# Performance work log

Hardware: AMD Instinct MI355X
Metric: run time of the kernel (lower is better)

The kernel has to match this reference:

```python
import jax, jax.numpy as jnp
import numpy as np

MUL = 128            # multiplicity of 0e and 1o node irreps
N_NODES = 10000
N_EDGES = 160000
R_BASIS = 8          # edge_feats_irreps.num_irreps
HIDDEN = 64
W_NUMEL = 4 * MUL    # conv_tp.weight_numel (4 uvu paths, edge mul = 1)
SQRT3 = 3.0 ** 0.5
SILU_2MOM = 1.679177   # e3nn normalize2mom constant for SiLU
AVG_NUM_NEIGHBORS = 10.0


def setup_inputs() -> dict:
    key = jax.random.key(0)
    ks = jax.random.split(key, 12)
    rn = lambda k, s: jax.random.normal(k, s, dtype=jnp.float32)
    return {
        "node_feats": rn(ks[0], (N_NODES, 4 * MUL)),        # 128x0e + 128x1o
        "edge_attrs": rn(ks[1], (N_EDGES, 4)),               # 1x0e + 1x1o spherical harmonics
        "edge_feats": rn(ks[2], (N_EDGES, R_BASIS)),         # 8x0e radial basis
        "edge_index": jax.random.randint(ks[3], (2, N_EDGES), 0, N_NODES),
        "W_up0": rn(ks[4], (MUL, MUL)),                      # linear_up, 0e block
        "W_up1": rn(ks[5], (MUL, MUL)),                      # linear_up, 1o block
        "W_mlp1": rn(ks[6], (R_BASIS, HIDDEN)),
        "W_mlp2": rn(ks[7], (HIDDEN, HIDDEN)),
        "W_mlp3": rn(ks[8], (HIDDEN, HIDDEN)),
        "W_mlp4": rn(ks[9], (HIDDEN, W_NUMEL)),
        "W_out0": rn(ks[10], (2 * MUL, MUL)),                # linear: 256x0e -> 128x0e
        "W_out1": rn(ks[11], (2 * MUL, MUL)),                # linear: 256x1o -> 128x1o
    }


def _lin_irreps(x0, x1, W0, W1):
    # equivariant o3.Linear: per-irrep channel mixing with 1/sqrt(fan_in)
    y0 = (x0 @ W0) / jnp.sqrt(jnp.float32(W0.shape[0]))
    y1 = jnp.einsum('num,uv->nvm', x1, W1) / jnp.sqrt(jnp.float32(W1.shape[0]))
    return y0, y1


def _forward(node_feats, edge_attrs, edge_feats, edge_index,
             W_up0, W_up1, W_mlp1, W_mlp2, W_mlp3, W_mlp4, W_out0, W_out1):
    num_nodes = node_feats.shape[0]
    sender, receiver = edge_index[0], edge_index[1]

    # split node feats into irrep blocks: [N,128] scalars, [N,128,3] vectors
    x0 = node_feats[:, :MUL]
    x1 = node_feats[:, MUL:].reshape(num_nodes, MUL, 3)
    x0, x1 = _lin_irreps(x0, x1, W_up0, W_up1)  # linear_up

    # radial MLP (e3nn FullyConnectedNet with normalized SiLU) -> per-edge TP weights
    h = edge_feats
    for W in (W_mlp1, W_mlp2, W_mlp3):
        h = SILU_2MOM * jax.nn.silu((h @ W) / jnp.sqrt(jnp.float32(W.shape[0])))
    tpw = (h @ W_mlp4) / jnp.sqrt(jnp.float32(W_mlp4.shape[0]))  # [E, 4*MUL]
    w1, w2, w3, w4 = jnp.split(tpw, 4, axis=-1)  # per-path [E, MUL]

    # gather sender features
    s0 = x0[sender]              # [E, MUL]
    s1 = x1[sender]              # [E, MUL, 3]
    y0 = edge_attrs[:, 0:1]      # [E, 1]  (0e sh)
    y1 = edge_attrs[:, 1:4]      # [E, 3]  (1o sh)

    # weighted uvu CG tensor product (component norm: alpha = sqrt(2l_out+1), w3j sum-sq = 1)
    p1 = w1 * s0 * y0                                    # 0e x 0e -> 0e  [E, MUL]
    p2 = (w2 * s0)[:, :, None] * y1[:, None, :]          # 0e x 1o -> 1o  [E, MUL, 3]
    p3 = w3[:, :, None] * s1 * y0[:, None, :]            # 1o x 0e -> 1o  [E, MUL, 3]
    p4 = w4 * jnp.einsum('eum,em->eu', s1, y1) / SQRT3   # 1o x 1o -> 0e  [E, MUL]

    # irreps_mid.simplify() = 256x0e + 256x1o
    m0 = jnp.concatenate([p1, p4], axis=-1)              # [E, 2*MUL]
    m1 = jnp.concatenate([p2, p3], axis=1)               # [E, 2*MUL, 3]

    # scatter-sum over receivers
    msg0 = jax.ops.segment_sum(m0, receiver, num_segments=num_nodes)
    msg1 = jax.ops.segment_sum(m1, receiver, num_segments=num_nodes)

    o0, o1 = _lin_irreps(msg0, msg1, W_out0, W_out1)
    out = jnp.concatenate([o0, o1.reshape(num_nodes, 3 * MUL)], axis=-1)
    return out / AVG_NUM_NEIGHBORS


def reference(node_feats, edge_attrs, edge_feats, edge_index,
              W_up0, W_up1, W_mlp1, W_mlp2, W_mlp3, W_mlp4, W_out0, W_out1):
    return _forward(node_feats, edge_attrs, edge_feats, edge_index,
                    W_up0, W_up1, W_mlp1, W_mlp2, W_mlp3, W_mlp4, W_out0, W_out1)
```

## Files before the change

### kernel.cpp

```cpp
#include <hip/hip_runtime.h>
#include <stdint.h>

#define NN 10000
#define NE 160000

typedef short short8 __attribute__((ext_vector_type(8)));
typedef float f32x4 __attribute__((ext_vector_type(4)));

__device__ __forceinline__ float bf2f(unsigned short u) {
    return __uint_as_float(((uint32_t)u) << 16);
}
__device__ __forceinline__ float bflo(uint32_t u) { return __uint_as_float(u << 16); }
__device__ __forceinline__ float bfhi(uint32_t u) { return __uint_as_float(u & 0xffff0000u); }
__device__ __forceinline__ unsigned short f2bf(float f) {
    uint32_t u = __float_as_uint(f);
    u += 0x7fffu + ((u >> 16) & 1u);
    return (unsigned short)(u >> 16);
}
__device__ __forceinline__ uint32_t pack2(float lo, float hi) {
    return (uint32_t)f2bf(lo) | ((uint32_t)f2bf(hi) << 16);
}
__device__ __forceinline__ float silu2(float x) {
    return 1.679177f * x / (1.f + __expf(-x));
}

__global__ __launch_bounds__(256) void k_wup(const float* __restrict__ Wu0,
                                             const float* __restrict__ Wu1,
                                             unsigned short* __restrict__ w0T,
                                             unsigned short* __restrict__ w1T) {
    const float s = 0.08838834764831845f;
    for (int i = threadIdx.x + blockIdx.x * 256; i < 16384; i += 256 * 64) {
        int u = i >> 7, v = i & 127;
        w0T[v * 128 + u] = f2bf(Wu0[i] * s);
        w1T[v * 128 + u] = f2bf(Wu1[i] * s);
    }
}

__global__ __launch_bounds__(256) void k_prep(const float* __restrict__ nf,
                                              unsigned short* __restrict__ x0b,
                                              unsigned short* __restrict__ x1b) {
    int idx = blockIdx.x * 256 + threadIdx.x;
    int n = idx >> 7, u = idx & 127;
    const float* row = nf + (size_t)n * 512;
    x0b[(size_t)n * 128 + u] = f2bf(row[u]);
    const float* p = row + 128 + u * 3;
    x1b[(size_t)n * 128 + u]                = f2bf(p[0]);
    x1b[1280000 + (size_t)n * 128 + u]      = f2bf(p[1]);
    x1b[2560000 + (size_t)n * 128 + u]      = f2bf(p[2]);
}

__global__ __launch_bounds__(256) void k_upg(const unsigned short* __restrict__ x0b,
                                             const unsigned short* __restrict__ x1b,
                                             const unsigned short* __restrict__ w0T,
                                             const unsigned short* __restrict__ w1T,
                                             float* __restrict__ xw) {
    int wave = threadIdx.x >> 6, lane = threadIdx.x & 63;
    int wid = blockIdx.x * 4 + wave;
    if (wid >= 1250) return;
    int tile = wid >> 1, half = wid & 1;
    int n0 = tile * 16;
    int lm = lane & 15, lq = lane >> 4;

    uint4 A0[4], A1[3][4];
    const unsigned short* a0r = x0b + (size_t)(n0 + lm) * 128 + lq * 8;
#pragma unroll
    for (int kf = 0; kf < 4; ++kf) A0[kf] = *(const uint4*)(a0r + kf * 32);
#pragma unroll
    for (int m = 0; m < 3; ++m) {
        const unsigned short* a1r = x1b + 1280000 * (size_t)m + (size_t)(n0 + lm) * 128 + lq * 8;
#pragma unroll
        for (int kf = 0; kf < 4; ++kf) A1[m][kf] = *(const uint4*)(a1r + kf * 32);
    }

    for (int vq = 0; vq < 4; ++vq) {
        int vt = half * 4 + vq;
        const unsigned short* b0r = w0T + (vt * 16 + lm) * 128 + lq * 8;
        const unsigned short* b1r = w1T + (vt * 16 + lm) * 128 + lq * 8;
        f32x4 acc0 = {0.f, 0.f, 0.f, 0.f};
#pragma unroll
        for (int kf = 0; kf < 4; ++kf) {
            short8 b = __builtin_bit_cast(short8, *(const uint4*)(b0r + kf * 32));
            acc0 = __builtin_amdgcn_mfma_f32_16x16x32_bf16(
                __builtin_bit_cast(short8, A0[kf]), b, acc0, 0, 0, 0);
        }
        f32x4 acc1[3];
#pragma unroll
        for (int m = 0; m < 3; ++m) acc1[m] = (f32x4){0.f, 0.f, 0.f, 0.f};
#pragma unroll
        for (int kf = 0; kf < 4; ++kf) {
            short8 b = __builtin_bit_cast(short8, *(const uint4*)(b1r + kf * 32));
#pragma unroll
            for (int m = 0; m < 3; ++m)
                acc1[m] = __builtin_amdgcn_mfma_f32_16x16x32_bf16(
                    __builtin_bit_cast(short8, A1[m][kf]), b, acc1[m], 0, 0, 0);
        }
        int col = vt * 16 + lm;
#pragma unroll
        for (int r = 0; r < 4; ++r) {
            float* o = xw + (size_t)(n0 + lq * 4 + r) * 512;
            o[col] = acc0[r];
            o[128 + col] = acc1[0][r];
            o[256 + col] = acc1[1][r];
            o[384 + col] = acc1[2][r];
        }
    }
}

__global__ __launch_bounds__(256) void k_wmlp(const float* __restrict__ W1,
                                              const float* __restrict__ W2,
                                              const float* __restrict__ W3,
                                              unsigned short* __restrict__ w1Tp,
                                              unsigned short* __restrict__ w2T,
                                              unsigned short* __restrict__ w3T) {
    int t = threadIdx.x;
    for (int i = t; i < 2048; i += 256) {
        int jj = i >> 5, k = i & 31;
        w1Tp[i] = (k < 8) ? f2bf(W1[k * 64 + jj] * 0.3535533905932738f) : 0;
    }
    for (int i = t; i < 4096; i += 256) {
        int jj = i >> 6, k = i & 63;
        w2T[i] = f2bf(W2[k * 64 + jj] * 0.125f);
        w3T[i] = f2bf(W3[k * 64 + jj] * 0.125f);
    }
}

__global__ __launch_bounds__(256) void k_mlp(const float* __restrict__ ef,
                                             const unsigned short* __restrict__ w1Tp,
                                             const unsigned short* __restrict__ w2T,
                                             const unsigned short* __restrict__ w3T,
                                             unsigned short* __restrict__ h3w) {
    __shared__ __align__(16) unsigned short hs_all[4][16 * 72];
    int wave = threadIdx.x >> 6, lane = threadIdx.x & 63;
    int lm = lane & 15, lq = lane >> 4;
    int e0 = blockIdx.x * 64 + wave * 16;
    unsigned short* h = hs_all[wave];
    unsigned short* hrow = h + lm * 72;

    uint4 A1[4];
#pragma unroll
    for (int mt = 0; mt < 4; ++mt)
        A1[mt] = *(const uint4*)(w1Tp + (mt * 16 + lm) * 32 + lq * 8);
    uint4 b = {0, 0, 0, 0};
    if (lq == 0) {
        const float4* p = (const float4*)(ef + (size_t)(e0 + lm) * 8);
        float4 x = p[0], y = p[1];
        b.x = pack2(x.x, x.y); b.y = pack2(x.z, x.w);
        b.z = pack2(y.x, y.y); b.w = pack2(y.z, y.w);
    }
    short8 bb = __builtin_bit_cast(short8, b);
#pragma unroll
    for (int mt = 0; mt < 4; ++mt) {
        f32x4 acc = {0.f, 0.f, 0.f, 0.f};
        acc = __builtin_amdgcn_mfma_f32_16x16x32_bf16(
            __builtin_bit_cast(short8, A1[mt]), bb, acc, 0, 0, 0);
        uint2 v;
        v.x = pack2(silu2(acc[0]), silu2(acc[1]));
        v.y = pack2(silu2(acc[2]), silu2(acc[3]));
        *(uint2*)(hrow + mt * 16 + lq * 4) = v;
    }

    uint4 A2[4][2];
#pragma unroll
    for (int mt = 0; mt < 4; ++mt)
#pragma unroll
        for (int kf = 0; kf < 2; ++kf)
            A2[mt][kf] = *(const uint4*)(w2T + (mt * 16 + lm) * 64 + kf * 32 + lq * 8);
    {
        short8 B0 = __builtin_bit_cast(short8, *(const uint4*)(hrow + lq * 8));
        short8 B1 = __builtin_bit_cast(short8, *(const uint4*)(hrow + 32 + lq * 8));
#pragma unroll
        for (int mt = 0; mt < 4; ++mt) {
            f32x4 acc = {0.f, 0.f, 0.f, 0.f};
            acc = __builtin_amdgcn_mfma_f32_16x16x32_bf16(
                __builtin_bit_cast(short8, A2[mt][0]), B0, acc, 0, 0, 0);
            acc = __builtin_amdgcn_mfma_f32_16x16x32_bf16(
                __builtin_bit_cast(short8, A2[mt][1]), B1, acc, 0, 0, 0);
            uint2 v;
            v.x = pack2(silu2(acc[0]), silu2(acc[1]));
            v.y = pack2(silu2(acc[2]), silu2(acc[3]));
            *(uint2*)(hrow + mt * 16 + lq * 4) = v;
        }
    }

    uint4 A3[4][2];
#pragma unroll
    for (int mt = 0; mt < 4; ++mt)
#pragma unroll
        for (int kf = 0; kf < 2; ++kf)
            A3[mt][kf] = *(const uint4*)(w3T + (mt * 16 + lm) * 64 + kf * 32 + lq * 8);
    {
        short8 B0 = __builtin_bit_cast(short8, *(const uint4*)(hrow + lq * 8));
        short8 B1 = __builtin_bit_cast(short8, *(const uint4*)(hrow + 32 + lq * 8));
#pragma unroll
        for (int mt = 0; mt < 4; ++mt) {
            f32x4 acc = {0.f, 0.f, 0.f, 0.f};
            acc = __builtin_amdgcn_mfma_f32_16x16x32_bf16(
                __builtin_bit_cast(short8, A3[mt][0]), B0, acc, 0, 0, 0);
            acc = __builtin_amdgcn_mfma_f32_16x16x32_bf16(
                __builtin_bit_cast(short8, A3[mt][1]), B1, acc, 0, 0, 0);
            uint2 v;
            v.x = pack2(silu2(acc[0]), silu2(acc[1]));
            v.y = pack2(silu2(acc[2]), silu2(acc[3]));
            *(uint2*)(hrow + mt * 16 + lq * 4) = v;
        }
    }

#pragma unroll
    for (int q = 0; q < 2; ++q) {
        int c = lane + q * 64;
        int row = c >> 3, col = (c & 7) * 8;
        *(uint4*)(h3w + (size_t)(e0 + row) * 64 + col) =
            *(const uint4*)(h + row * 72 + col);
    }
}

__global__ void k_zero(int* __restrict__ p, int n) {
    int i = blockIdx.x * 256 + threadIdx.x;
    if (i < n) p[i] = 0;
}
__global__ void k_hist(const int* __restrict__ ei, int* __restrict__ counts) {
    int e = blockIdx.x * 256 + threadIdx.x;
    if (e < NE) atomicAdd(&counts[ei[NE + e]], 1);
}
__global__ __launch_bounds__(1024) void k_scan(const int* __restrict__ counts,
                                               int* __restrict__ offs,
                                               int* __restrict__ cursor) {
    __shared__ int sums[1024];
    int t = threadIdx.x;
    int base = t * 10;
    int s = 0;
    for (int i = 0; i < 10; ++i) {
        int idx = base + i;
        if (idx < NN) s += counts[idx];
    }
    sums[t] = s;
    __syncthreads();
    for (int d = 1; d < 1024; d <<= 1) {
        int v = (t >= d) ? sums[t - d] : 0;
        __syncthreads();
        if (t >= d) sums[t] += v;
        __syncthreads();
    }
    int run = (t == 0) ? 0 : sums[t - 1];
    for (int i = 0; i < 10; ++i) {
        int idx = base + i;
        if (idx < NN) {
            offs[idx] = run;
            cursor[idx] = run;
            run += counts[idx];
        }
    }
    if (t == 0) offs[NN] = NE;
}
__global__ void k_fill(const int* __restrict__ ei, int* __restrict__ cursor,
                       int* __restrict__ elist) {
    int e = blockIdx.x * 256 + threadIdx.x;
    if (e < NE) {
        int slot = atomicAdd(&cursor[ei[NE + e]], 1);
        elist[slot] = e;
    }
}
__global__ void k_gather(const int* __restrict__ ei, const float* __restrict__ ea,
                         const int* __restrict__ elist,
                         int* __restrict__ eis, float4* __restrict__ eap) {
    int i = blockIdx.x * 256 + threadIdx.x;
    if (i < NE) {
        int e = elist[i];
        eis[i] = ei[e];
        eap[i] = *(const float4*)(ea + (size_t)e * 4);
    }
}

__global__ void k_w4t(const float* __restrict__ W4, unsigned short* __restrict__ w4T) {
    int idx = blockIdx.x * 256 + threadIdx.x;
    int k = idx >> 9, c = idx & 511;
    w4T[c * 64 + k] = f2bf(W4[idx]);
}
__global__ void k_wt2(const float* __restrict__ Wo0, const float* __restrict__ Wo1,
                      unsigned short* __restrict__ woT0, unsigned short* __restrict__ woT1) {
    int idx = blockIdx.x * 256 + threadIdx.x;
    int u = idx >> 7, v = idx & 127;
    woT0[v * 256 + u] = f2bf(Wo0[idx]);
    woT1[v * 256 + u] = f2bf(Wo1[idx]);
}

__global__ __launch_bounds__(256) void k_tpw(const unsigned short* __restrict__ h3w,
                                             const unsigned short* __restrict__ w4T,
                                             const int* __restrict__ elist,
                                             unsigned short* __restrict__ tpw) {
    int wave = threadIdx.x >> 6, lane = threadIdx.x & 63;
    int e0 = blockIdx.x * 256 + wave * 64;
    int lm = lane & 15, lq = lane >> 4;
    uint4 B[4][2];
#pragma unroll
    for (int n = 0; n < 4; ++n) {
        int esrc = elist[e0 + n * 16 + lm];
#pragma unroll
        for (int k = 0; k < 2; ++k)
            B[n][k] = *(const uint4*)(h3w + (size_t)esrc * 64 + k * 32 + lq * 8);
    }
    const unsigned short* aw = w4T + lm * 64 + lq * 8;
#pragma unroll 2
    for (int m = 0; m < 32; ++m) {
        f32x4 acc0 = {0.f, 0.f, 0.f, 0.f};
        f32x4 acc1 = {0.f, 0.f, 0.f, 0.f};
        f32x4 acc2 = {0.f, 0.f, 0.f, 0.f};
        f32x4 acc3 = {0.f, 0.f, 0.f, 0.f};
#pragma unroll
        for (int k = 0; k < 2; ++k) {
            uint4 a_raw = *(const uint4*)(aw + m * 1024 + k * 32);
            short8 a = __builtin_bit_cast(short8, a_raw);
            acc0 = __builtin_amdgcn_mfma_f32_16x16x32_bf16(a, __builtin_bit_cast(short8, B[0][k]), acc0, 0, 0, 0);
            acc1 = __builtin_amdgcn_mfma_f32_16x16x32_bf16(a, __builtin_bit_cast(short8, B[1][k]), acc1, 0, 0, 0);
            acc2 = __builtin_amdgcn_mfma_f32_16x16x32_bf16(a, __builtin_bit_cast(short8, B[2][k]), acc2, 0, 0, 0);
            acc3 = __builtin_amdgcn_mfma_f32_16x16x32_bf16(a, __builtin_bit_cast(short8, B[3][k]), acc3, 0, 0, 0);
        }
        int cb = m * 16 + lq * 4;
        int plane = cb >> 7, cl = cb & 127;
        unsigned short* pb = tpw + (size_t)plane * NE * 128 + cl;
        uint2 v;
        v.x = pack2(acc0[0] * 0.125f, acc0[1] * 0.125f);
        v.y = pack2(acc0[2] * 0.125f, acc0[3] * 0.125f);
        *(uint2*)(pb + (size_t)(e0 + 0 * 16 + lm) * 128) = v;
        v.x = pack2(acc1[0] * 0.125f, acc1[1] * 0.125f);
        v.y = pack2(acc1[2] * 0.125f, acc1[3] * 0.125f);
        *(uint2*)(pb + (size_t)(e0 + 1 * 16 + lm) * 128) = v;
        v.x = pack2(acc2[0] * 0.125f, acc2[1] * 0.125f);
        v.y = pack2(acc2[2] * 0.125f, acc2[3] * 0.125f);
        *(uint2*)(pb + (size_t)(e0 + 2 * 16 + lm) * 128) = v;
        v.x = pack2(acc3[0] * 0.125f, acc3[1] * 0.125f);
        v.y = pack2(acc3[2] * 0.125f, acc3[3] * 0.125f);
        *(uint2*)(pb + (size_t)(e0 + 3 * 16 + lm) * 128) = v;
    }
}

__global__ __launch_bounds__(256) void k_msg2(const float* __restrict__ xw,
                                              const unsigned short* __restrict__ tpw,
                                              const int* __restrict__ eis,
                                              const float4* __restrict__ eap,
                                              const int* __restrict__ offs,
                                              unsigned short* __restrict__ msgb) {
    int n = blockIdx.x, t = threadIdx.x;
    int j = t >> 6, c0 = (t & 63) * 2;
    int beg = offs[n], end = offs[n + 1];
    const unsigned short* plane = tpw + (size_t)j * NE * 128;
    float a0 = 0.f, a1 = 0.f, a2 = 0.f, a3 = 0.f, a4 = 0.f, a5 = 0.f;

    if (end > beg) {
        const int last = end - 1;
        int s[8];
#pragma unroll
        for (int k = 0; k < 8; ++k) {
            int idx = beg + k;
            s[k] = eis[idx <= last ? idx : last];
        }
        if (j == 0) {
            for (int g = beg; g < end; g += 8) {
                int sn[8];
#pragma unroll
                for (int k = 0; k < 8; ++k) {
                    int idx = g + 8 + k;
                    sn[k] = eis[idx <= last ? idx : last];
                }
                float wa[8], wb[8], ey[8];
                float2 x[8];
#pragma unroll
                for (int k = 0; k < 8; ++k) {
                    int idx = g + k;
                    int cl = idx <= last ? idx : last;
                    uint32_t w = *(const uint32_t*)(plane + (size_t)cl * 128 + c0);
                    wa[k] = idx <= last ? bflo(w) : 0.f;
                    wb[k] = idx <= last ? bfhi(w) : 0.f;
                    ey[k] = eap[cl].x;
                    x[k] = *(const float2*)(xw + (size_t)s[k] * 512 + c0);
                }
#pragma unroll
                for (int k = 0; k < 8; ++k) {
                    a0 += wa[k] * x[k].x * ey[k];
                    a1 += wb[k] * x[k].y * ey[k];
                }
#pragma unroll
                for (int k = 0; k < 8; ++k) s[k] = sn[k];
            }
        } else if (j == 1) {
            for (int g = beg; g < end; g += 8) {
                int sn[8];
#pragma unroll
                for (int k = 0; k < 8; ++k) {
                    int idx = g + 8 + k;
                    sn[k] = eis[idx <= last ? idx : last];
                }
                float wa[8], wb[8], ex[8], ey[8], ez[8];
                float2 x[8];
#pragma unroll
                for (int k = 0; k < 8; ++k) {
                    int idx = g + k;
                    int cl = idx <= last ? idx : last;
                    uint32_t w = *(const uint32_t*)(plane + (size_t)cl * 128 + c0);
                    wa[k] = idx <= last ? bflo(w) : 0.f;
                    wb[k] = idx <= last ? bfhi(w) : 0.f;
                    float4 e = eap[cl];
                    ex[k] = e.y; ey[k] = e.z; ez[k] = e.w;
                    x[k] = *(const float2*)(xw + (size_t)s[k] * 512 + c0);
                }
#pragma unroll
                for (int k = 0; k < 8; ++k) {
                    float ta = wa[k] * x[k].x, tb = wb[k] * x[k].y;
                    a0 += ta * ex[k]; a1 += ta * ey[k]; a2 += ta * ez[k];
                    a3 += tb * ex[k]; a4 += tb * ey[k]; a5 += tb * ez[k];
                }
#pragma unroll
                for (int k = 0; k < 8; ++k) s[k] = sn[k];
            }
        } else if (j == 2) {
            for (int g = beg; g < end; g += 8) {
                int sn[8];
#pragma unroll
                for (int k = 0; k < 8; ++k) {
                    int idx = g + 8 + k;
                    sn[k] = eis[idx <= last ? idx : last];
                }
                float wa[8], wb[8], ey[8];
                float2 x0[8], x1[8], x2[8];
#pragma unroll
                for (int k = 0; k < 8; ++k) {
                    int idx = g + k;
                    int cl = idx <= last ? idx : last;
                    uint32_t w = *(const uint32_t*)(plane + (size_t)cl * 128 + c0);
                    wa[k] = idx <= last ? bflo(w) : 0.f;
                    wb[k] = idx <= last ? bfhi(w) : 0.f;
                    ey[k] = eap[cl].x;
                    const float* xr = xw + (size_t)s[k] * 512 + c0;
                    x0[k] = *(const float2*)(xr + 128);
                    x1[k] = *(const float2*)(xr + 256);
                    x2[k] = *(const float2*)(xr + 384);
                }
#pragma unroll
                for (int k = 0; k < 8; ++k) {
                    float f0 = wa[k] * ey[k], f1 = wb[k] * ey[k];
                    a0 += f0 * x0[k].x; a1 += f0 * x1[k].x; a2 += f0 * x2[k].x;
                    a3 += f1 * x0[k].y; a4 += f1 * x1[k].y; a5 += f1 * x2[k].y;
                }
#pragma unroll
                for (int k = 0; k < 8; ++k) s[k] = sn[k];
            }
        } else {
            for (int g = beg; g < end; g += 8) {
                int sn[8];
#pragma unroll
                for (int k = 0; k < 8; ++k) {
                    int idx = g + 8 + k;
                    sn[k] = eis[idx <= last ? idx : last];
                }
                float wa[8], wb[8], ex[8], ey[8], ez[8];
                float2 x0[8], x1[8], x2[8];
#pragma unroll
                for (int k = 0; k < 8; ++k) {
                    int idx = g + k;
                    int cl = idx <= last ? idx : last;
                    uint32_t w = *(const uint32_t*)(plane + (size_t)cl * 128 + c0);
                    wa[k] = idx <= last ? bflo(w) : 0.f;
                    wb[k] = idx <= last ? bfhi(w) : 0.f;
                    float4 e = eap[cl];
                    ex[k] = e.y; ey[k] = e.z; ez[k] = e.w;
                    const float* xr = xw + (size_t)s[k] * 512 + c0;
                    x0[k] = *(const float2*)(xr + 128);
                    x1[k] = *(const float2*)(xr + 256);
                    x2[k] = *(const float2*)(xr + 384);
                }
#pragma unroll
                for (int k = 0; k < 8; ++k) {
                    float dta = x0[k].x * ex[k] + x1[k].x * ey[k] + x2[k].x * ez[k];
                    float dtb = x0[k].y * ex[k] + x1[k].y * ey[k] + x2[k].y * ez[k];
                    a0 += wa[k] * dta * 0.5773502691896258f;
                    a1 += wb[k] * dtb * 0.5773502691896258f;
                }
#pragma unroll
                for (int k = 0; k < 8; ++k) s[k] = sn[k];
            }
        }
    }

    unsigned short* mr = msgb + (size_t)n * 1024;
    if (j == 0) {
        *(uint32_t*)(mr + c0) = pack2(a0, a1);
    } else if (j == 1) {
        *(uint32_t*)(mr + 256 + c0)       = pack2(a0, a3);
        *(uint32_t*)(mr + 256 + 256 + c0) = pack2(a1, a4);
        *(uint32_t*)(mr + 256 + 512 + c0) = pack2(a2, a5);
    } else if (j == 2) {
        *(uint32_t*)(mr + 256 + 128 + c0)       = pack2(a0, a3);
        *(uint32_t*)(mr + 256 + 256 + 128 + c0) = pack2(a1, a4);
        *(uint32_t*)(mr + 256 + 512 + 128 + c0) = pack2(a2, a5);
    } else {
        *(uint32_t*)(mr + 128 + c0) = pack2(a0, a1);
    }
}

__global__ __launch_bounds__(256) void k_out0(const unsigned short* __restrict__ msgb,
                                              const unsigned short* __restrict__ woT,
                                              float* __restrict__ out) {
    int wave = threadIdx.x >> 6, lane = threadIdx.x & 63;
    int wid = blockIdx.x * 4 + wave;
    if (wid >= NN / 16) return;
    int n0 = wid * 16;
    int lm = lane & 15, lq = lane >> 4;
    uint4 A[8];
    const unsigned short* ar = msgb + (size_t)(n0 + lm) * 1024 + lq * 8;
#pragma unroll
    for (int kf = 0; kf < 8; ++kf) A[kf] = *(const uint4*)(ar + kf * 32);
    const unsigned short* br = woT + lm * 256 + lq * 8;
    float* ob = out + (size_t)n0 * 512;
    for (int vt = 0; vt < 8; ++vt) {
        f32x4 acc = {0.f, 0.f, 0.f, 0.f};
#pragma unroll
        for (int kf = 0; kf < 8; ++kf) {
            uint4 b = *(const uint4*)(br + vt * 16 * 256 + kf * 32);
            acc = __builtin_amdgcn_mfma_f32_16x16x32_bf16(
                __builtin_bit_cast(short8, A[kf]), __builtin_bit_cast(short8, b), acc, 0, 0, 0);
        }
#pragma unroll
        for (int r = 0; r < 4; ++r)
            ob[(size_t)(lq * 4 + r) * 512 + vt * 16 + lm] = acc[r] * 0.00625f;
    }
}

__global__ __launch_bounds__(256) void k_out1(const unsigned short* __restrict__ msgb,
                                              const unsigned short* __restrict__ woT,
                                              float* __restrict__ out) {
    int wave = threadIdx.x >> 6, lane = threadIdx.x & 63;
    int wid = blockIdx.x * 4 + wave;
    if (wid >= NN / 16) return;
    int n0 = wid * 16;
    int lm = lane & 15, lq = lane >> 4;
    uint4 A[3][8];
    const unsigned short* ar = msgb + (size_t)(n0 + lm) * 1024 + 256 + lq * 8;
#pragma unroll
    for (int m = 0; m < 3; ++m)
#pragma unroll
        for (int kf = 0; kf < 8; ++kf)
            A[m][kf] = *(const uint4*)(ar + m * 256 + kf * 32);
    const unsigned short* br = woT + lm * 256 + lq * 8;
    float* ob = out + (size_t)n0 * 512 + 128;
    for (int vt = 0; vt < 8; ++vt) {
        f32x4 acc[3];
#pragma unroll
        for (int m = 0; m < 3; ++m) acc[m] = (f32x4){0.f, 0.f, 0.f, 0.f};
#pragma unroll
        for (int kf = 0; kf < 8; ++kf) {
            uint4 braw = *(const uint4*)(br + vt * 16 * 256 + kf * 32);
            short8 b = __builtin_bit_cast(short8, braw);
#pragma unroll
            for (int m = 0; m < 3; ++m)
                acc[m] = __builtin_amdgcn_mfma_f32_16x16x32_bf16(
                    __builtin_bit_cast(short8, A[m][kf]), b, acc[m], 0, 0, 0);
        }
        int vb = (vt * 16 + lm) * 3;
#pragma unroll
        for (int r = 0; r < 4; ++r) {
            float* o = ob + (size_t)(lq * 4 + r) * 512 + vb;
            o[0] = acc[0][r] * 0.00625f;
            o[1] = acc[1][r] * 0.00625f;
            o[2] = acc[2][r] * 0.00625f;
        }
    }
}

extern "C" void kernel_launch(void* const* d_in, const int* in_sizes, int n_in,
                              void* d_out, int out_size, void* d_ws, size_t ws_size,
                              hipStream_t stream) {
    const float* nf  = (const float*)d_in[0];
    const float* ea  = (const float*)d_in[1];
    const float* ef  = (const float*)d_in[2];
    const int*   ei  = (const int*)d_in[3];
    const float* Wu0 = (const float*)d_in[4];
    const float* Wu1 = (const float*)d_in[5];
    const float* W1  = (const float*)d_in[6];
    const float* W2  = (const float*)d_in[7];
    const float* W3  = (const float*)d_in[8];
    const float* W4  = (const float*)d_in[9];
    const float* Wo0 = (const float*)d_in[10];
    const float* Wo1 = (const float*)d_in[11];
    float* out = (float*)d_out;
    char* ws = (char*)d_ws;

    unsigned short* tpw  = (unsigned short*)ws;
    unsigned short* x0b  = (unsigned short*)ws;
    unsigned short* x1b  = (unsigned short*)(ws + 2560000);
    float*          xw   = (float*)(ws + 163840000);
    unsigned short* h3w  = (unsigned short*)(ws + 184320000);
    unsigned short* woT0 = (unsigned short*)(ws + 184320000);
    unsigned short* woT1 = (unsigned short*)(ws + 184320000 + 65536);
    float4*         eap  = (float4*)(ws + 184320000 + 131072);
    int*            eis  = (int*)(ws + 184320000 + 131072 + 2560000);
    unsigned short* msgb = (unsigned short*)(ws + 204800000);
    unsigned short* w4T  = (unsigned short*)(ws + 225280000);
    int* ib     = (int*)(ws + 225280000 + 65536);
    int* counts = ib;
    int* offs   = ib + 10240;
    int* cursor = ib + 20480;
    int* elist  = ib + 30720;
    unsigned short* w1Tp = (unsigned short*)(ws + 226108416);
    unsigned short* w2T  = (unsigned short*)(ws + 226108416 + 4096);
    unsigned short* w3T  = (unsigned short*)(ws + 226108416 + 12288);
    unsigned short* w0T  = (unsigned short*)(ws + 226128896);
    unsigned short* w1T  = (unsigned short*)(ws + 226161664);

    k_wmlp <<<1, 256, 0, stream>>>(W1, W2, W3, w1Tp, w2T, w3T);
    k_wup  <<<64, 256, 0, stream>>>(Wu0, Wu1, w0T, w1T);
    k_prep <<<5000, 256, 0, stream>>>(nf, x0b, x1b);
    k_upg  <<<313, 256, 0, stream>>>(x0b, x1b, w0T, w1T, xw);
    k_mlp  <<<2500, 256, 0, stream>>>(ef, w1Tp, w2T, w3T, h3w);
    k_w4t  <<<128, 256, 0, stream>>>(W4, w4T);
    k_zero <<<40, 256, 0, stream>>>(counts, NN);
    k_hist <<<625, 256, 0, stream>>>(ei, counts);
    k_scan <<<1, 1024, 0, stream>>>(counts, offs, cursor);
    k_fill <<<625, 256, 0, stream>>>(ei, cursor, elist);
    k_tpw  <<<625, 256, 0, stream>>>(h3w, w4T, elist, tpw);
    k_wt2  <<<128, 256, 0, stream>>>(Wo0, Wo1, woT0, woT1);
    k_gather<<<625, 256, 0, stream>>>(ei, ea, elist, eis, eap);
    k_msg2 <<<NN, 256, 0, stream>>>(xw, tpw, eis, eap, offs, msgb);
    k_out0 <<<157, 256, 0, stream>>>(msgb, woT0, out);
    k_out1 <<<157, 256, 0, stream>>>(msgb, woT1, out);
}
```

Before: 351.8 us.

## Fuse per-edge tensor-product weight GEMM into the message aggregation kernel

```diff
diff --git a/kernel.cpp b/kernel.cpp
--- a/kernel.cpp
+++ b/kernel.cpp
@@ -284,199 +284,170 @@
     woT1[v * 256 + u] = f2bf(Wo1[idx]);
 }
 
-__global__ __launch_bounds__(256) void k_tpw(const unsigned short* __restrict__ h3w,
-                                             const unsigned short* __restrict__ w4T,
-                                             const int* __restrict__ elist,
-                                             unsigned short* __restrict__ tpw) {
-    int wave = threadIdx.x >> 6, lane = threadIdx.x & 63;
-    int e0 = blockIdx.x * 256 + wave * 64;
-    int lm = lane & 15, lq = lane >> 4;
-    uint4 B[4][2];
-#pragma unroll
-    for (int n = 0; n < 4; ++n) {
-        int esrc = elist[e0 + n * 16 + lm];
-#pragma unroll
-        for (int k = 0; k < 2; ++k)
-            B[n][k] = *(const uint4*)(h3w + (size_t)esrc * 64 + k * 32 + lq * 8);
-    }
-    const unsigned short* aw = w4T + lm * 64 + lq * 8;
-#pragma unroll 2
-    for (int m = 0; m < 32; ++m) {
-        f32x4 acc0 = {0.f, 0.f, 0.f, 0.f};
-        f32x4 acc1 = {0.f, 0.f, 0.f, 0.f};
-        f32x4 acc2 = {0.f, 0.f, 0.f, 0.f};
-        f32x4 acc3 = {0.f, 0.f, 0.f, 0.f};
-#pragma unroll
-        for (int k = 0; k < 2; ++k) {
-            uint4 a_raw = *(const uint4*)(aw + m * 1024 + k * 32);
-            short8 a = __builtin_bit_cast(short8, a_raw);
-            acc0 = __builtin_amdgcn_mfma_f32_16x16x32_bf16(a, __builtin_bit_cast(short8, B[0][k]), acc0, 0, 0, 0);
-            acc1 = __builtin_amdgcn_mfma_f32_16x16x32_bf16(a, __builtin_bit_cast(short8, B[1][k]), acc1, 0, 0, 0);
-            acc2 = __builtin_amdgcn_mfma_f32_16x16x32_bf16(a, __builtin_bit_cast(short8, B[2][k]), acc2, 0, 0, 0);
-            acc3 = __builtin_amdgcn_mfma_f32_16x16x32_bf16(a, __builtin_bit_cast(short8, B[3][k]), acc3, 0, 0, 0);
-        }
-        int cb = m * 16 + lq * 4;
-        int plane = cb >> 7, cl = cb & 127;
-        unsigned short* pb = tpw + (size_t)plane * NE * 128 + cl;
-        uint2 v;
-        v.x = pack2(acc0[0] * 0.125f, acc0[1] * 0.125f);
-        v.y = pack2(acc0[2] * 0.125f, acc0[3] * 0.125f);
-        *(uint2*)(pb + (size_t)(e0 + 0 * 16 + lm) * 128) = v;
-        v.x = pack2(acc1[0] * 0.125f, acc1[1] * 0.125f);
-        v.y = pack2(acc1[2] * 0.125f, acc1[3] * 0.125f);
-        *(uint2*)(pb + (size_t)(e0 + 1 * 16 + lm) * 128) = v;
-        v.x = pack2(acc2[0] * 0.125f, acc2[1] * 0.125f);
-        v.y = pack2(acc2[2] * 0.125f, acc2[3] * 0.125f);
-        *(uint2*)(pb + (size_t)(e0 + 2 * 16 + lm) * 128) = v;
-        v.x = pack2(acc3[0] * 0.125f, acc3[1] * 0.125f);
-        v.y = pack2(acc3[2] * 0.125f, acc3[3] * 0.125f);
-        *(uint2*)(pb + (size_t)(e0 + 3 * 16 + lm) * 128) = v;
-    }
-}
-
 __global__ __launch_bounds__(256) void k_msg2(const float* __restrict__ xw,
-                                              const unsigned short* __restrict__ tpw,
+                                              const unsigned short* __restrict__ h3w,
+                                              const unsigned short* __restrict__ w4T,
                                               const int* __restrict__ eis,
                                               const float4* __restrict__ eap,
                                               const int* __restrict__ offs,
+                                              const int* __restrict__ elist,
                                               unsigned short* __restrict__ msgb) {
+    __shared__ __align__(16) float wl_all[4][16][132];
     int n = blockIdx.x, t = threadIdx.x;
-    int j = t >> 6, c0 = (t & 63) * 2;
+    int j = t >> 6, lw = t & 63;
+    int lm = lw & 15, lq = lw >> 4;
+    int c0 = lw * 2;
     int beg = offs[n], end = offs[n + 1];
-    const unsigned short* plane = tpw + (size_t)j * NE * 128;
+    float (*wl)[132] = wl_all[j];
     float a0 = 0.f, a1 = 0.f, a2 = 0.f, a3 = 0.f, a4 = 0.f, a5 = 0.f;
 
     if (end > beg) {
         const int last = end - 1;
-        int s[8];
-#pragma unroll
-        for (int k = 0; k < 8; ++k) {
-            int idx = beg + k;
-            s[k] = eis[idx <= last ? idx : last];
-        }
-        if (j == 0) {
-            for (int g = beg; g < end; g += 8) {
-                int sn[8];
-#pragma unroll
-                for (int k = 0; k < 8; ++k) {
-                    int idx = g + 8 + k;
-                    sn[k] = eis[idx <= last ? idx : last];
+        uint4 A[8][2];
+        const unsigned short* aw = w4T + (size_t)(j * 8 * 16 + lm) * 64 + lq * 8;
+#pragma unroll
+        for (int mt = 0; mt < 8; ++mt)
+#pragma unroll
+            for (int kf = 0; kf < 2; ++kf)
+                A[mt][kf] = *(const uint4*)(aw + mt * 1024 + kf * 32);
+
+        for (int cbeg = beg; cbeg < end; cbeg += 16) {
+            int slot = cbeg + lm;
+            slot = slot <= last ? slot : last;
+            int esrc = elist[slot];
+            const unsigned short* hr = h3w + (size_t)esrc * 64 + lq * 8;
+            short8 B0 = __builtin_bit_cast(short8, *(const uint4*)(hr));
+            short8 B1 = __builtin_bit_cast(short8, *(const uint4*)(hr + 32));
+#pragma unroll
+            for (int mt = 0; mt < 8; ++mt) {
+                f32x4 acc = {0.f, 0.f, 0.f, 0.f};
+                acc = __builtin_amdgcn_mfma_f32_16x16x32_bf16(
+                    __builtin_bit_cast(short8, A[mt][0]), B0, acc, 0, 0, 0);
+                acc = __builtin_amdgcn_mfma_f32_16x16x32_bf16(
+                    __builtin_bit_cast(short8, A[mt][1]), B1, acc, 0, 0, 0);
+                acc = acc * 0.125f;
+                *(f32x4*)&wl[lm][mt * 16 + lq * 4] = acc;
+            }
+
+            int cend = cbeg + 16 < end ? cbeg + 16 : end;
+            if (j == 0) {
+                for (int g = cbeg; g < cend; g += 8) {
+                    int s_[8]; float wa[8], wb[8], ey[8]; float2 x[8];
+#pragma unroll
+                    for (int k = 0; k < 8; ++k) {
+                        int idx = g + k;
+                        int cl = idx <= last ? idx : last;
+                        s_[k] = eis[cl];
+                    }
+#pragma unroll
+                    for (int k = 0; k < 8; ++k) {
+                        int idx = g + k;
+                        int cl = idx <= last ? idx : last;
+                        int e = idx - cbeg;
+                        float2 wv = *(const float2*)&wl[e][c0];
+                        wa[k] = idx <= last ? wv.x : 0.f;
+                        wb[k] = idx <= last ? wv.y : 0.f;
+                        ey[k] = eap[cl].x;
+                        x[k] = *(const float2*)(xw + (size_t)s_[k] * 512 + c0);
+                    }
+#pragma unroll
+                    for (int k = 0; k < 8; ++k) {
+                        a0 += wa[k] * x[k].x * ey[k];
+                        a1 += wb[k] * x[k].y * ey[k];
+                    }
                 }
-                float wa[8], wb[8], ey[8];
-                float2 x[8];
-#pragma unroll
-                for (int k = 0; k < 8; ++k) {
-                    int idx = g + k;
-                    int cl = idx <= last ? idx : last;
-                    uint32_t w = *(const uint32_t*)(plane + (size_t)cl * 128 + c0);
-                    wa[k] = idx <= last ? bflo(w) : 0.f;
-                    wb[k] = idx <= last ? bfhi(w) : 0.f;
-                    ey[k] = eap[cl].x;
-                    x[k] = *(const float2*)(xw + (size_t)s[k] * 512 + c0);
+            } else if (j == 1) {
+                for (int g = cbeg; g < cend; g += 8) {
+                    int s_[8]; float wa[8], wb[8], ex[8], ey[8], ez[8]; float2 x[8];
+#pragma unroll
+                    for (int k = 0; k < 8; ++k) {
+                        int idx = g + k;
+                        int cl = idx <= last ? idx : last;
+                        s_[k] = eis[cl];
+                    }
+#pragma unroll
+                    for (int k = 0; k < 8; ++k) {
+                        int idx = g + k;
+                        int cl = idx <= last ? idx : last;
+                        int e = idx - cbeg;
+                        float2 wv = *(const float2*)&wl[e][c0];
+                        wa[k] = idx <= last ? wv.x : 0.f;
+                        wb[k] = idx <= last ? wv.y : 0.f;
+                        float4 ev = eap[cl];
+                        ex[k] = ev.y; ey[k] = ev.z; ez[k] = ev.w;
+                        x[k] = *(const float2*)(xw + (size_t)s_[k] * 512 + c0);
+                    }
+#pragma unroll
+                    for (int k = 0; k < 8; ++k) {
+                        float ta = wa[k] * x[k].x, tb = wb[k] * x[k].y;
+                        a0 += ta * ex[k]; a1 += ta * ey[k]; a2 += ta * ez[k];
+                        a3 += tb * ex[k]; a4 += tb * ey[k]; a5 += tb * ez[k];
+                    }
                 }
-#pragma unroll
-                for (int k = 0; k < 8; ++k) {
-                    a0 += wa[k] * x[k].x * ey[k];
-                    a1 += wb[k] * x[k].y * ey[k];
+            } else if (j == 2) {
+                for (int g = cbeg; g < cend; g += 8) {
+                    int s_[8]; float wa[8], wb[8], ey[8];
+                    float2 x0[8], x1[8], x2[8];
+#pragma unroll
+                    for (int k = 0; k < 8; ++k) {
+                        int idx = g + k;
+                        int cl = idx <= last ? idx : last;
+                        s_[k] = eis[cl];
+                    }
+#pragma unroll
+                    for (int k = 0; k < 8; ++k) {
+                        int idx = g + k;
+                        int cl = idx <= last ? idx : last;
+                        int e = idx - cbeg;
+                        float2 wv = *(const float2*)&wl[e][c0];
+                        wa[k] = idx <= last ? wv.x : 0.f;
+                        wb[k] = idx <= last ? wv.y : 0.f;
+                        ey[k] = eap[cl].x;
+                        const float* xr = xw + (size_t)s_[k] * 512 + c0;
+                        x0[k] = *(const float2*)(xr + 128);
+                        x1[k] = *(const float2*)(xr + 256);
+                        x2[k] = *(const float2*)(xr + 384);
+                    }
+#pragma unroll
+                    for (int k = 0; k < 8; ++k) {
+                        float f0 = wa[k] * ey[k], f1 = wb[k] * ey[k];
+                        a0 += f0 * x0[k].x; a1 += f0 * x1[k].x; a2 += f0 * x2[k].x;
+                        a3 += f1 * x0[k].y; a4 += f1 * x1[k].y; a5 += f1 * x2[k].y;
+                    }
                 }
-#pragma unroll
-                for (int k = 0; k < 8; ++k) s[k] = sn[k];
-            }
-        } else if (j == 1) {
-            for (int g = beg; g < end; g += 8) {
-                int sn[8];
-#pragma unroll
-                for (int k = 0; k < 8; ++k) {
-                    int idx = g + 8 + k;
-                    sn[k] = eis[idx <= last ? idx : last];
+            } else {
+                for (int g = cbeg; g < cend; g += 8) {
+                    int s_[8]; float wa[8], wb[8], ex[8], ey[8], ez[8];
+                    float2 x0[8], x1[8], x2[8];
+#pragma unroll
+                    for (int k = 0; k < 8; ++k) {
+                        int idx = g + k;
+                        int cl = idx <= last ? idx : last;
+                        s_[k] = eis[cl];
+                    }
+#pragma unroll
+                    for (int k = 0; k < 8; ++k) {
+                        int idx = g + k;
+                        int cl = idx <= last ? idx : last;
+                        int e = idx - cbeg;
+                        float2 wv = *(const float2*)&wl[e][c0];
+                        wa[k] = idx <= last ? wv.x : 0.f;
+                        wb[k] = idx <= last ? wv.y : 0.f;
+                        float4 ev = eap[cl];
+                        ex[k] = ev.y; ey[k] = ev.z; ez[k] = ev.w;
+                        const float* xr = xw + (size_t)s_[k] * 512 + c0;
+                        x0[k] = *(const float2*)(xr + 128);
+                        x1[k] = *(const float2*)(xr + 256);
+                        x2[k] = *(const float2*)(xr + 384);
+                    }
+#pragma unroll
+                    for (int k = 0; k < 8; ++k) {
+                        float dta = x0[k].x * ex[k] + x1[k].x * ey[k] + x2[k].x * ez[k];
+                        float dtb = x0[k].y * ex[k] + x1[k].y * ey[k] + x2[k].y * ez[k];
+                        a0 += wa[k] * dta * 0.5773502691896258f;
+                        a1 += wb[k] * dtb * 0.5773502691896258f;
+                    }
                 }
-                float wa[8], wb[8], ex[8], ey[8], ez[8];
-                float2 x[8];
-#pragma unroll
-                for (int k = 0; k < 8; ++k) {
-                    int idx = g + k;
-                    int cl = idx <= last ? idx : last;
-                    uint32_t w = *(const uint32_t*)(plane + (size_t)cl * 128 + c0);
-                    wa[k] = idx <= last ? bflo(w) : 0.f;
-                    wb[k] = idx <= last ? bfhi(w) : 0.f;
-                    float4 e = eap[cl];
-                    ex[k] = e.y; ey[k] = e.z; ez[k] = e.w;
-                    x[k] = *(const float2*)(xw + (size_t)s[k] * 512 + c0);
-                }
-#pragma unroll
-                for (int k = 0; k < 8; ++k) {
-                    float ta = wa[k] * x[k].x, tb = wb[k] * x[k].y;
-                    a0 += ta * ex[k]; a1 += ta * ey[k]; a2 += ta * ez[k];
-                    a3 += tb * ex[k]; a4 += tb * ey[k]; a5 += tb * ez[k];
-                }
-#pragma unroll
-                for (int k = 0; k < 8; ++k) s[k] = sn[k];
-            }
-        } else if (j == 2) {
-            for (int g = beg; g < end; g += 8) {
-                int sn[8];
-#pragma unroll
-                for (int k = 0; k < 8; ++k) {
-                    int idx = g + 8 + k;
-                    sn[k] = eis[idx <= last ? idx : last];
-                }
-                float wa[8], wb[8], ey[8];
-                float2 x0[8], x1[8], x2[8];
-#pragma unroll
-                for (int k = 0; k < 8; ++k) {
-                    int idx = g + k;
-                    int cl = idx <= last ? idx : last;
-                    uint32_t w = *(const uint32_t*)(plane + (size_t)cl * 128 + c0);
-                    wa[k] = idx <= last ? bflo(w) : 0.f;
-                    wb[k] = idx <= last ? bfhi(w) : 0.f;
-                    ey[k] = eap[cl].x;
-                    const float* xr = xw + (size_t)s[k] * 512 + c0;
-                    x0[k] = *(const float2*)(xr + 128);
-                    x1[k] = *(const float2*)(xr + 256);
-                    x2[k] = *(const float2*)(xr + 384);
-                }
-#pragma unroll
-                for (int k = 0; k < 8; ++k) {
-                    float f0 = wa[k] * ey[k], f1 = wb[k] * ey[k];
-                    a0 += f0 * x0[k].x; a1 += f0 * x1[k].x; a2 += f0 * x2[k].x;
-                    a3 += f1 * x0[k].y; a4 += f1 * x1[k].y; a5 += f1 * x2[k].y;
-                }
-#pragma unroll
-                for (int k = 0; k < 8; ++k) s[k] = sn[k];
-            }
-        } else {
-            for (int g = beg; g < end; g += 8) {
-                int sn[8];
-#pragma unroll
-                for (int k = 0; k < 8; ++k) {
-                    int idx = g + 8 + k;
-                    sn[k] = eis[idx <= last ? idx : last];
-                }
-                float wa[8], wb[8], ex[8], ey[8], ez[8];
-                float2 x0[8], x1[8], x2[8];
-#pragma unroll
-                for (int k = 0; k < 8; ++k) {
-                    int idx = g + k;
-                    int cl = idx <= last ? idx : last;
-                    uint32_t w = *(const uint32_t*)(plane + (size_t)cl * 128 + c0);
-                    wa[k] = idx <= last ? bflo(w) : 0.f;
-                    wb[k] = idx <= last ? bfhi(w) : 0.f;
-                    float4 e = eap[cl];
-                    ex[k] = e.y; ey[k] = e.z; ez[k] = e.w;
-                    const float* xr = xw + (size_t)s[k] * 512 + c0;
-                    x0[k] = *(const float2*)(xr + 128);
-                    x1[k] = *(const float2*)(xr + 256);
-                    x2[k] = *(const float2*)(xr + 384);
-                }
-#pragma unroll
-                for (int k = 0; k < 8; ++k) {
-                    float dta = x0[k].x * ex[k] + x1[k].x * ey[k] + x2[k].x * ez[k];
-                    float dtb = x0[k].y * ex[k] + x1[k].y * ey[k] + x2[k].y * ez[k];
-                    a0 += wa[k] * dta * 0.5773502691896258f;
-                    a1 += wb[k] * dtb * 0.5773502691896258f;
-                }
-#pragma unroll
-                for (int k = 0; k < 8; ++k) s[k] = sn[k];
             }
         }
     }
@@ -584,15 +555,14 @@
     float* out = (float*)d_out;
     char* ws = (char*)d_ws;
 
-    unsigned short* tpw  = (unsigned short*)ws;
     unsigned short* x0b  = (unsigned short*)ws;
     unsigned short* x1b  = (unsigned short*)(ws + 2560000);
+    unsigned short* woT0 = (unsigned short*)ws;
+    unsigned short* woT1 = (unsigned short*)(ws + 65536);
+    float4*         eap  = (float4*)(ws + 131072);
+    int*            eis  = (int*)(ws + 131072 + 2560000);
     float*          xw   = (float*)(ws + 163840000);
     unsigned short* h3w  = (unsigned short*)(ws + 184320000);
-    unsigned short* woT0 = (unsigned short*)(ws + 184320000);
-    unsigned short* woT1 = (unsigned short*)(ws + 184320000 + 65536);
-    float4*         eap  = (float4*)(ws + 184320000 + 131072);
-    int*            eis  = (int*)(ws + 184320000 + 131072 + 2560000);
     unsigned short* msgb = (unsigned short*)(ws + 204800000);
     unsigned short* w4T  = (unsigned short*)(ws + 225280000);
     int* ib     = (int*)(ws + 225280000 + 65536);
@@ -616,10 +586,9 @@
     k_hist <<<625, 256, 0, stream>>>(ei, counts);
     k_scan <<<1, 1024, 0, stream>>>(counts, offs, cursor);
     k_fill <<<625, 256, 0, stream>>>(ei, cursor, elist);
-    k_tpw  <<<625, 256, 0, stream>>>(h3w, w4T, elist, tpw);
     k_wt2  <<<128, 256, 0, stream>>>(Wo0, Wo1, woT0, woT1);
     k_gather<<<625, 256, 0, stream>>>(ei, ea, elist, eis, eap);
-    k_msg2 <<<NN, 256, 0, stream>>>(xw, tpw, eis, eap, offs, msgb);
+    k_msg2 <<<NN, 256, 0, stream>>>(xw, h3w, w4T, eis, eap, offs, elist, msgb);
     k_out0 <<<157, 256, 0, stream>>>(msgb, woT0, out);
     k_out1 <<<157, 256, 0, stream>>>(msgb, woT1, out);
 }
```

Result: no change. 356.7 us (+1.4%).
